# Kernel tuning notes

Hardware: AMD Instinct MI355X
Metric: run time of the kernel (lower is better)

## Reference

```python
import jax, jax.numpy as jnp
import numpy as np


def _linear_init(key, fan_in, fan_out):
    bound = 1.0 / np.sqrt(fan_in)
    k1, k2 = jax.random.split(key)
    w = jax.random.uniform(k1, (fan_in, fan_out), jnp.float32, -bound, bound)
    b = jax.random.uniform(k2, (fan_out,), jnp.float32, -bound, bound)
    return w, b


def setup_inputs() -> dict:
    key = jax.random.key(0)
    ks = jax.random.split(key, 8)
    B, T, K, F, H, D = 4, 64, 50, 6, 128, 256
    states = jax.random.normal(ks[0], (B, T, K, F), jnp.float32)
    masks = (jax.random.uniform(ks[1], (B, T, K)) < 0.9).astype(jnp.float32)
    w_a, b_a = _linear_init(ks[2], F, H)              # agent_encoder
    w_r1, b_r1 = _linear_init(ks[3], 2 * H + 3, H)    # relation_encoder layer 1
    w_r2, b_r2 = _linear_init(ks[4], H, H)            # relation_encoder layer 2
    w_g, b_g = _linear_init(ks[5], 2 * H, H)          # graph_aggregation
    w_f1, b_f1 = _linear_init(ks[6], H, D)            # final_encoder layer 1
    w_f2, b_f2 = _linear_init(ks[7], D, D)            # final_encoder layer 2
    return dict(states=states, masks=masks, w_a=w_a, b_a=b_a,
                w_r1=w_r1, b_r1=b_r1, w_r2=w_r2, b_r2=b_r2,
                w_g=w_g, b_g=b_g, w_f1=w_f1, b_f1=b_f1, w_f2=w_f2, b_f2=b_f2)


def _safe_norm(r):
    # sqrt(sum r^2) with well-defined gradient at 0 (torch.norm convention)
    sq = jnp.sum(r * r, axis=-1, keepdims=True)
    return jnp.where(sq == 0, 0.0, jnp.sqrt(jnp.where(sq == 0, 1.0, sq)))


def reference(states, masks, w_a, b_a, w_r1, b_r1, w_r2, b_r2,
              w_g, b_g, w_f1, b_f1, w_f2, b_f2):
    B, T, K, F = states.shape
    H = w_a.shape[1]
    s = states.reshape(B * T, K, F)            # [N,K,F]
    m = masks.reshape(B * T, K)                # [N,K]
    agent_feat = jax.nn.relu(s @ w_a + b_a)    # [N,K,H] (dropout = identity, eval)
    pos = s[..., :2]
    vel = s[..., 2:4]
    # rel[n,i,j] = quantity_j - quantity_i
    rel_pos = pos[:, None, :, :] - pos[:, :, None, :]   # [N,K,K,2]
    rel_vel = vel[:, None, :, :] - vel[:, :, None, :]
    dist = _safe_norm(rel_pos)                          # [N,K,K,1]
    rx, ry = rel_pos[..., 0:1], rel_pos[..., 1:2]
    safe_x = jnp.where((rx == 0) & (ry == 0), 1.0, rx)  # atan2(0,1)=atan2(0,0)=0
    angle = jnp.arctan2(ry, safe_x)
    speed_diff = _safe_norm(rel_vel)
    geo = jnp.concatenate([dist, angle, speed_diff], axis=-1)  # [N,K,K,3]
    # Split the first relation linear instead of materializing the
    # [N,K,K,2H+3] concat: cat([f_i, f_j, geo]) @ w_r1 == f@w_i + f@w_j + geo@w_geo
    x_i = agent_feat @ w_r1[:H]            # [N,K,H]
    x_j = agent_feat @ w_r1[H:2 * H]       # [N,K,H]
    g = geo @ w_r1[2 * H:] + b_r1          # [N,K,K,H]
    h = jax.nn.relu(x_i[:, :, None, :] + x_j[:, None, :, :] + g)
    rel_feat = h @ w_r2 + b_r2             # [N,K,K,H]
    mask_pairs = m[:, :, None] * m[:, None, :]          # [N,i,j]
    rel_feat = rel_feat * mask_pairs[..., None]
    denom = jnp.maximum(mask_pairs.sum(axis=2, keepdims=True), 1.0)  # [N,K,1]
    agg = rel_feat.sum(axis=2) / denom                  # [N,K,H]
    combined = jax.nn.relu(agent_feat @ w_g[:H] + agg @ w_g[H:] + b_g)  # [N,K,H]
    me = m[..., None]
    pooled = (combined * me).sum(axis=1) / jnp.maximum(me.sum(axis=1), 1.0)  # [N,H]
    latent = jax.nn.relu(pooled @ w_f1 + b_f1) @ w_f2 + b_f2                 # [N,D]
    return latent.reshape(B, T, -1)
```

## Files before the change

kernel.cpp:

```cpp
#include <hip/hip_runtime.h>

#define KA 50
#define KP 52
#define H 128
#define D 256
#define NBLK 256
#define BLOCK 1024
#define NG 8
#define RPT 7
#define STRD 136

#define WS_WI 0
#define WS_WJ 32
#define WS_WR2 64
#define WS_WG 96
#define NFRAG 160

typedef __attribute__((ext_vector_type(8))) short bf16x8;
typedef __attribute__((ext_vector_type(4))) float f32x4;

__device__ __forceinline__ float bf2f(unsigned short u) {
  return __uint_as_float(((unsigned)u) << 16);
}
__device__ __forceinline__ unsigned short f2bf(float f) {
  unsigned u = __float_as_uint(f);
  u = (u + 0x7FFFu + ((u >> 16) & 1u)) >> 16;
  return (unsigned short)u;
}
__device__ __forceinline__ float rlf(float v, int l) {
  return __int_as_float(__builtin_amdgcn_readlane(__float_as_int(v), l));
}

__global__ void pack_weights(const float* __restrict__ w_r1,
                             const float* __restrict__ w_r2,
                             const float* __restrict__ w_g,
                             unsigned short* __restrict__ wp) {
  const int t = blockIdx.x * 256 + threadIdx.x;
  if (t >= NFRAG * 64) return;
  const int f = t >> 6, lane = t & 63;
  const float* W; int rowbase, sf;
  if (f < 64)       { W = w_r1; rowbase = (f < 32) ? 0 : 128; sf = f & 31; }
  else if (f < 96)  { W = w_r2; rowbase = 0; sf = f - 64; }
  else              { W = w_g;  rowbase = 0; sf = f - 96; }
  const int kt = sf >> 3, ctl = sf & 7;
  const int col = ctl * 16 + (lane & 15);
  const int k0  = rowbase + kt * 32 + (lane >> 4) * 8;
  unsigned short v[8];
  #pragma unroll
  for (int j = 0; j < 8; ++j) v[j] = f2bf(W[(k0 + j) * H + col]);
  #pragma unroll
  for (int j = 0; j < 8; ++j) wp[(size_t)t * 8 + j] = v[j];
}

struct alignas(16) Smem {
  unsigned short af[KP * STRD];
  unsigned short xi[KP * STRD];
  unsigned short xj[KP * H];
  unsigned short hsum[KP * STRD];
  float red[1024];
  float pooled[H];
  float latent1[D];
  float s[KA][6];
  float m[64];
  float cnta[KP];
  float invden[KP];
  float cnt;
};

__global__ void __launch_bounds__(BLOCK) rpe_kernel(
    const float* __restrict__ states, const float* __restrict__ masks,
    const float* __restrict__ w_a,  const float* __restrict__ b_a,
    const float* __restrict__ w_r1, const float* __restrict__ b_r1,
    const float* __restrict__ b_r2,
    const float* __restrict__ b_g,
    const float* __restrict__ w_f1, const float* __restrict__ b_f1,
    const float* __restrict__ w_f2, const float* __restrict__ b_f2,
    const unsigned short* __restrict__ wp,
    float* __restrict__ out) {
  __shared__ Smem sh;
  const int n = blockIdx.x;
  const int tid = threadIdx.x;
  const int c = tid & (H - 1);
  const int bg = tid >> 7;
  const int wid = tid >> 6, lane = tid & 63;
  const int ct = wid & 7;
  const int rtb = (wid >> 3) * 2;
  const int fr = lane & 15;
  const int fkg = lane >> 4;
  const int col = ct * 16 + fr;

  const float bac = b_a[c];
  const float wa0 = w_a[0*H+c], wa1 = w_a[1*H+c], wa2 = w_a[2*H+c];
  const float wa3 = w_a[3*H+c], wa4 = w_a[4*H+c], wa5 = w_a[5*H+c];
  const int c0 = 2 * lane;
  const float wgd0  = w_r1[256*H + c0], wgd1  = w_r1[256*H + c0+1];
  const float wgan0 = w_r1[257*H + c0], wgan1 = w_r1[257*H + c0+1];
  const float wgs0  = w_r1[258*H + c0], wgs1  = w_r1[258*H + c0+1];
  const float br10  = b_r1[c0],         br11  = b_r1[c0+1];

  {
    if (tid < KA * 6) ((float*)sh.s)[tid] = states[(size_t)n * (KA * 6) + tid];
    if (tid < 64) sh.m[tid] = (tid < KA) ? masks[(size_t)n * KA + tid] : 0.f;
    if (tid < 2 * H) {
      const int r5 = KA + (tid >> 7), cc = tid & (H - 1);
      sh.af[r5 * STRD + cc] = 0;
      sh.hsum[r5 * STRD + cc] = 0;
    }
  }
  __syncthreads();
  if (wid == 0) {
    float v = sh.m[lane];
    v += __shfl_xor(v, 1);  v += __shfl_xor(v, 2);  v += __shfl_xor(v, 4);
    v += __shfl_xor(v, 8);  v += __shfl_xor(v, 16); v += __shfl_xor(v, 32);
    if (lane == 0) sh.cnt = v;
  }

  const int bl = (lane < KA) ? lane : (KA - 1);
  const float pbx = sh.s[bl][0], pby = sh.s[bl][1];
  const float pvx = sh.s[bl][2], pvy = sh.s[bl][3];
  const float mb  = sh.m[lane];
  float dG[3], aG[3], sG[3];
  #pragma unroll
  for (int r = 0; r < 3; ++r) {
    const int ar = wid + 16 * r;
    const float rx  = pbx - sh.s[ar][0], ry  = pby - sh.s[ar][1];
    const float dvx = pvx - sh.s[ar][2], dvy = pvy - sh.s[ar][3];
    dG[r] = sqrtf(fmaf(rx, rx, ry * ry));
    const float sx = (rx == 0.f && ry == 0.f) ? 1.f : rx;
    aG[r] = atan2f(ry, sx);
    sG[r] = sqrtf(fmaf(dvx, dvx, dvy * dvy));
  }
  float dGt = 0.f, aGt = 0.f, sGt = 0.f;
  if (wid < 2) {
    const int ar = 48 + wid;
    const float rx  = pbx - sh.s[ar][0], ry  = pby - sh.s[ar][1];
    const float dvx = pvx - sh.s[ar][2], dvy = pvy - sh.s[ar][3];
    dGt = sqrtf(fmaf(rx, rx, ry * ry));
    const float sx = (rx == 0.f && ry == 0.f) ? 1.f : rx;
    aGt = atan2f(ry, sx);
    sGt = sqrtf(fmaf(dvx, dvx, dvy * dvy));
  }

  {
    #pragma unroll
    for (int r = 0; r < RPT; ++r) {
      const int a = bg + NG * r;
      if (a < KA) {
        const float* srow = sh.s[a];
        float v = fmaf(srow[0], wa0, fmaf(srow[1], wa1, fmaf(srow[2], wa2,
                  fmaf(srow[3], wa3, fmaf(srow[4], wa4, fmaf(srow[5], wa5, bac))))));
        sh.af[a * STRD + c] = f2bf(fmaxf(v, 0.f));
      }
    }
  }
  bf16x8 Bi[4], Bj[4];
  #pragma unroll
  for (int kt = 0; kt < 4; ++kt) {
    Bi[kt] = *(const bf16x8*)&wp[(size_t)((WS_WI + kt*8 + ct) * 64 + lane) * 8];
    Bj[kt] = *(const bf16x8*)&wp[(size_t)((WS_WJ + kt*8 + ct) * 64 + lane) * 8];
  }
  __syncthreads();
  if (tid < KP) {
    const float ca = (tid < KA) ? sh.m[tid] * sh.cnt : 0.f;
    sh.cnta[tid] = ca;
    sh.invden[tid] = 1.0f / fmaxf(ca, 1.0f);
  }

  {
    f32x4 ci0 = {0,0,0,0}, ci1 = {0,0,0,0}, cj0 = {0,0,0,0}, cj1 = {0,0,0,0};
    #pragma unroll
    for (int kt = 0; kt < 4; ++kt) {
      const bf16x8 A0 = *(const bf16x8*)&sh.af[(rtb*16 + fr) * STRD + kt*32 + fkg*8];
      const bf16x8 A1 = *(const bf16x8*)&sh.af[((rtb+1)*16 + fr) * STRD + kt*32 + fkg*8];
      ci0 = __builtin_amdgcn_mfma_f32_16x16x32_bf16(A0, Bi[kt], ci0, 0, 0, 0);
      ci1 = __builtin_amdgcn_mfma_f32_16x16x32_bf16(A1, Bi[kt], ci1, 0, 0, 0);
      cj0 = __builtin_amdgcn_mfma_f32_16x16x32_bf16(A0, Bj[kt], cj0, 0, 0, 0);
      cj1 = __builtin_amdgcn_mfma_f32_16x16x32_bf16(A1, Bj[kt], cj1, 0, 0, 0);
    }
    #pragma unroll
    for (int rt2 = 0; rt2 < 2; ++rt2) {
      const f32x4 vi = rt2 ? ci1 : ci0;
      const f32x4 vj = rt2 ? cj1 : cj0;
      #pragma unroll
      for (int g = 0; g < 4; ++g) {
        const int r = (rtb + rt2) * 16 + fkg * 4 + g;
        if (r < KP) {
          sh.xi[r * STRD + col] = f2bf(vi[g]);
          sh.xj[r * H + col]    = f2bf(vj[g]);
        }
      }
    }
  }
  __syncthreads();

  {
    float b0v[3], b1v[3], h0v[3], h1v[3];
    #pragma unroll
    for (int r = 0; r < 3; ++r) {
      const int ar = wid + 16 * r;
      const unsigned xip = *(const unsigned*)&sh.xi[ar * STRD + c0];
      b0v[r] = bf2f((unsigned short)xip) + br10;
      b1v[r] = bf2f((unsigned short)(xip >> 16)) + br11;
      h0v[r] = 0.f; h1v[r] = 0.f;
    }
    #pragma unroll 10
    for (int b = 0; b < KA; ++b) {
      const unsigned xjp = *(const unsigned*)&sh.xj[b * H + c0];
      const float xj0 = __uint_as_float(xjp << 16);
      const float xj1 = __uint_as_float(xjp & 0xFFFF0000u);
      const float mm = rlf(mb, b);
      #pragma unroll
      for (int r = 0; r < 3; ++r) {
        const float dd = rlf(dG[r], b), aa = rlf(aG[r], b), ss = rlf(sG[r], b);
        float t0 = fmaf(dd, wgd0, b0v[r]); t0 = fmaf(aa, wgan0, t0);
        t0 = fmaf(ss, wgs0, t0);  t0 += xj0;
        float t1 = fmaf(dd, wgd1, b1v[r]); t1 = fmaf(aa, wgan1, t1);
        t1 = fmaf(ss, wgs1, t1);  t1 += xj1;
        h0v[r] = fmaf(mm, fmaxf(t0, 0.f), h0v[r]);
        h1v[r] = fmaf(mm, fmaxf(t1, 0.f), h1v[r]);
      }
    }
    #pragma unroll
    for (int r = 0; r < 3; ++r) {
      const int ar = wid + 16 * r;
      const float ma = sh.m[ar];
      const float g0 = h0v[r] * ma, g1 = h1v[r] * ma;
      *(unsigned*)&sh.hsum[ar * STRD + c0] =
          (unsigned)f2bf(g0) | ((unsigned)f2bf(g1) << 16);
    }
    if (wid < 2) {
      const int ar = 48 + wid;
      const unsigned xip = *(const unsigned*)&sh.xi[ar * STRD + c0];
      const float b0t = bf2f((unsigned short)xip) + br10;
      const float b1t = bf2f((unsigned short)(xip >> 16)) + br11;
      float h0 = 0.f, h1 = 0.f;
      #pragma unroll 10
      for (int b = 0; b < KA; ++b) {
        const unsigned xjp = *(const unsigned*)&sh.xj[b * H + c0];
        const float xj0 = __uint_as_float(xjp << 16);
        const float xj1 = __uint_as_float(xjp & 0xFFFF0000u);
        const float mm = rlf(mb, b);
        const float dd = rlf(dGt, b), aa = rlf(aGt, b), ss = rlf(sGt, b);
        float t0 = fmaf(dd, wgd0, b0t); t0 = fmaf(aa, wgan0, t0);
        t0 = fmaf(ss, wgs0, t0);  t0 += xj0;
        float t1 = fmaf(dd, wgd1, b1t); t1 = fmaf(aa, wgan1, t1);
        t1 = fmaf(ss, wgs1, t1);  t1 += xj1;
        h0 = fmaf(mm, fmaxf(t0, 0.f), h0);
        h1 = fmaf(mm, fmaxf(t1, 0.f), h1);
      }
      const float ma = sh.m[ar];
      const float g0 = h0 * ma, g1 = h1 * ma;
      *(unsigned*)&sh.hsum[ar * STRD + c0] =
          (unsigned)f2bf(g0) | ((unsigned)f2bf(g1) << 16);
    }
  }
  __syncthreads();

  f32x4 p0 = {0,0,0,0}, p1 = {0,0,0,0};
  {
    f32x4 a0 = {0,0,0,0}, a1 = {0,0,0,0};
    #pragma unroll
    for (int kt = 0; kt < 4; ++kt) {
      const bf16x8 B4 = *(const bf16x8*)&wp[(size_t)((WS_WR2 + kt*8 + ct) * 64 + lane) * 8];
      const bf16x8 A0h = *(const bf16x8*)&sh.hsum[(rtb*16 + fr) * STRD + kt*32 + fkg*8];
      const bf16x8 A1h = *(const bf16x8*)&sh.hsum[((rtb+1)*16 + fr) * STRD + kt*32 + fkg*8];
      a0 = __builtin_amdgcn_mfma_f32_16x16x32_bf16(A0h, B4, a0, 0, 0, 0);
      a1 = __builtin_amdgcn_mfma_f32_16x16x32_bf16(A1h, B4, a1, 0, 0, 0);
      const bf16x8 B5 = *(const bf16x8*)&wp[(size_t)((WS_WG + kt*8 + ct) * 64 + lane) * 8];
      const bf16x8 A0a = *(const bf16x8*)&sh.af[(rtb*16 + fr) * STRD + kt*32 + fkg*8];
      const bf16x8 A1a = *(const bf16x8*)&sh.af[((rtb+1)*16 + fr) * STRD + kt*32 + fkg*8];
      p0 = __builtin_amdgcn_mfma_f32_16x16x32_bf16(A0a, B5, p0, 0, 0, 0);
      p1 = __builtin_amdgcn_mfma_f32_16x16x32_bf16(A1a, B5, p1, 0, 0, 0);
    }
    const float br2c = b_r2[col];
    #pragma unroll
    for (int rt2 = 0; rt2 < 2; ++rt2) {
      const f32x4 v = rt2 ? a1 : a0;
      #pragma unroll
      for (int g = 0; g < 4; ++g) {
        const int r = (rtb + rt2) * 16 + fkg * 4 + g;
        if (r < KP) {
          const float val = fmaf(sh.cnta[r], br2c, v[g]) * sh.invden[r];
          sh.xi[r * STRD + col] = f2bf(val);
        }
      }
    }
  }
  __syncthreads();

  {
    #pragma unroll
    for (int kt = 0; kt < 4; ++kt) {
      const bf16x8 B = *(const bf16x8*)&wp[(size_t)((WS_WG + (kt+4)*8 + ct) * 64 + lane) * 8];
      const bf16x8 A0 = *(const bf16x8*)&sh.xi[(rtb*16 + fr) * STRD + kt*32 + fkg*8];
      const bf16x8 A1 = *(const bf16x8*)&sh.xi[((rtb+1)*16 + fr) * STRD + kt*32 + fkg*8];
      p0 = __builtin_amdgcn_mfma_f32_16x16x32_bf16(A0, B, p0, 0, 0, 0);
      p1 = __builtin_amdgcn_mfma_f32_16x16x32_bf16(A1, B, p1, 0, 0, 0);
    }
    const float bgc = b_g[col];
    float pv = 0.f;
    #pragma unroll
    for (int rt2 = 0; rt2 < 2; ++rt2) {
      const f32x4 v = rt2 ? p1 : p0;
      #pragma unroll
      for (int g = 0; g < 4; ++g) {
        const int r = (rtb + rt2) * 16 + fkg * 4 + g;
        if (r < KA) {
          pv = fmaf(sh.m[r], fmaxf(v[g] + bgc, 0.f), pv);
        }
      }
    }
    pv += __shfl_xor(pv, 16);
    pv += __shfl_xor(pv, 32);
    if (lane < 16) sh.red[(wid >> 3) * H + col] = pv;
  }
  const int d67 = tid & (D - 1);
  const int hh67 = tid >> 8;
  float wf1r[32];
  {
    const float* wf = w_f1 + d67;
    const int k06 = hh67 * 32;
    #pragma unroll
    for (int k = 0; k < 32; ++k) wf1r[k] = wf[(k06 + k) * D];
  }
  __syncthreads();
  if (tid < H) {
    const float invp = 1.0f / fmaxf(sh.cnt, 1.0f);
    sh.pooled[tid] = (sh.red[tid] + sh.red[H + tid]) * invp;
  }
  __syncthreads();

  {
    float acc = 0.f;
    const int k06 = hh67 * 32;
    #pragma unroll
    for (int k = 0; k < 32; ++k)
      acc = fmaf(sh.pooled[k06 + k], wf1r[k], acc);
    sh.red[hh67 * D + d67] = acc;
  }
  float wf2r[64];
  {
    const float* wf = w_f2 + d67;
    const int k07 = hh67 * 64;
    #pragma unroll
    for (int k = 0; k < 64; ++k) wf2r[k] = wf[(k07 + k) * D];
  }
  __syncthreads();
  if (tid < D) {
    sh.latent1[tid] = fmaxf(sh.red[tid] + sh.red[D + tid] +
                            sh.red[2*D + tid] + sh.red[3*D + tid] +
                            b_f1[tid], 0.f);
  }
  __syncthreads();

  {
    float acc = 0.f;
    const int k07 = hh67 * 64;
    #pragma unroll
    for (int k = 0; k < 64; ++k)
      acc = fmaf(sh.latent1[k07 + k], wf2r[k], acc);
    sh.red[hh67 * D + d67] = acc;
  }
  __syncthreads();
  if (tid < D) {
    out[(size_t)n * D + tid] = sh.red[tid] + sh.red[D + tid] +
                               sh.red[2*D + tid] + sh.red[3*D + tid] +
                               b_f2[tid];
  }
}

extern "C" void kernel_launch(void* const* d_in, const int* in_sizes, int n_in,
                              void* d_out, int out_size, void* d_ws, size_t ws_size,
                              hipStream_t stream) {
  const float* states = (const float*)d_in[0];
  const float* masks  = (const float*)d_in[1];
  const float* w_a  = (const float*)d_in[2];
  const float* b_a  = (const float*)d_in[3];
  const float* w_r1 = (const float*)d_in[4];
  const float* b_r1 = (const float*)d_in[5];
  const float* w_r2 = (const float*)d_in[6];
  const float* b_r2 = (const float*)d_in[7];
  const float* w_g  = (const float*)d_in[8];
  const float* b_g  = (const float*)d_in[9];
  const float* w_f1 = (const float*)d_in[10];
  const float* b_f1 = (const float*)d_in[11];
  const float* w_f2 = (const float*)d_in[12];
  const float* b_f2 = (const float*)d_in[13];
  float* out = (float*)d_out;
  unsigned short* wp = (unsigned short*)d_ws;

  hipLaunchKernelGGL(pack_weights, dim3((NFRAG * 64 + 255) / 256), dim3(256), 0, stream,
                     w_r1, w_r2, w_g, wp);
  hipLaunchKernelGGL(rpe_kernel, dim3(NBLK), dim3(BLOCK), 0, stream,
                     states, masks, w_a, b_a, w_r1, b_r1, b_r2,
                     b_g, w_f1, b_f1, w_f2, b_f2, wp, out);
}
```

Measured before the change: 42.59 us.

## Pack geometry into bf16 pairs, vectorize pair loop, drop weight prefetch registers

The pairwise relation loop now packs dist, angle, speed-diff and mask into two bf16-packed 32-bit values per row. That halves the readlane broadcasts per iteration (two instead of four per row), and the math is rewritten as 2-wide float vectors so the compiler can emit packed FMA/max. The final MLP no longer preloads w_f1/w_f2 columns into 32 and 64 registers ahead of barriers; it reads them from global inside partially unrolled loops. This lowers register pressure, but the geometry terms lose precision to bf16 and the weight-load latency is no longer hidden behind the barriers.

```diff
diff --git a/kernel.cpp b/kernel.cpp
--- a/kernel.cpp
+++ b/kernel.cpp
@@ -18,6 +18,7 @@
 
 typedef __attribute__((ext_vector_type(8))) short bf16x8;
 typedef __attribute__((ext_vector_type(4))) float f32x4;
+typedef __attribute__((ext_vector_type(2))) float v2f;
 
 __device__ __forceinline__ float bf2f(unsigned short u) {
   return __uint_as_float(((unsigned)u) << 16);
@@ -27,8 +28,8 @@
   u = (u + 0x7FFFu + ((u >> 16) & 1u)) >> 16;
   return (unsigned short)u;
 }
-__device__ __forceinline__ float rlf(float v, int l) {
-  return __int_as_float(__builtin_amdgcn_readlane(__float_as_int(v), l));
+__device__ __forceinline__ int rli(int v, int l) {
+  return __builtin_amdgcn_readlane(v, l);
 }
 
 __global__ void pack_weights(const float* __restrict__ w_r1,
@@ -93,10 +94,10 @@
   const float wa0 = w_a[0*H+c], wa1 = w_a[1*H+c], wa2 = w_a[2*H+c];
   const float wa3 = w_a[3*H+c], wa4 = w_a[4*H+c], wa5 = w_a[5*H+c];
   const int c0 = 2 * lane;
-  const float wgd0  = w_r1[256*H + c0], wgd1  = w_r1[256*H + c0+1];
-  const float wgan0 = w_r1[257*H + c0], wgan1 = w_r1[257*H + c0+1];
-  const float wgs0  = w_r1[258*H + c0], wgs1  = w_r1[258*H + c0+1];
-  const float br10  = b_r1[c0],         br11  = b_r1[c0+1];
+  const v2f wgd01  = { w_r1[256*H + c0], w_r1[256*H + c0+1] };
+  const v2f wgan01 = { w_r1[257*H + c0], w_r1[257*H + c0+1] };
+  const v2f wgs01  = { w_r1[258*H + c0], w_r1[258*H + c0+1] };
+  const v2f br101  = { b_r1[c0], b_r1[c0+1] };
 
   {
     if (tid < KA * 6) ((float*)sh.s)[tid] = states[(size_t)n * (KA * 6) + tid];
@@ -118,27 +119,31 @@
   const int bl = (lane < KA) ? lane : (KA - 1);
   const float pbx = sh.s[bl][0], pby = sh.s[bl][1];
   const float pvx = sh.s[bl][2], pvy = sh.s[bl][3];
-  const float mb  = sh.m[lane];
-  float dG[3], aG[3], sG[3];
+  const unsigned mbits = (sh.m[lane] != 0.f) ? 0x3F800000u : 0u;
+  unsigned q0[3], q1[3];
   #pragma unroll
   for (int r = 0; r < 3; ++r) {
     const int ar = wid + 16 * r;
     const float rx  = pbx - sh.s[ar][0], ry  = pby - sh.s[ar][1];
     const float dvx = pvx - sh.s[ar][2], dvy = pvy - sh.s[ar][3];
-    dG[r] = sqrtf(fmaf(rx, rx, ry * ry));
+    const float dist = sqrtf(fmaf(rx, rx, ry * ry));
     const float sx = (rx == 0.f && ry == 0.f) ? 1.f : rx;
-    aG[r] = atan2f(ry, sx);
-    sG[r] = sqrtf(fmaf(dvx, dvx, dvy * dvy));
-  }
-  float dGt = 0.f, aGt = 0.f, sGt = 0.f;
+    const float ang = atan2f(ry, sx);
+    const float sd  = sqrtf(fmaf(dvx, dvx, dvy * dvy));
+    q0[r] = (unsigned)f2bf(dist) | ((unsigned)f2bf(ang) << 16);
+    q1[r] = (unsigned)f2bf(sd) | mbits;
+  }
+  unsigned q0t = 0, q1t = 0;
   if (wid < 2) {
     const int ar = 48 + wid;
     const float rx  = pbx - sh.s[ar][0], ry  = pby - sh.s[ar][1];
     const float dvx = pvx - sh.s[ar][2], dvy = pvy - sh.s[ar][3];
-    dGt = sqrtf(fmaf(rx, rx, ry * ry));
+    const float dist = sqrtf(fmaf(rx, rx, ry * ry));
     const float sx = (rx == 0.f && ry == 0.f) ? 1.f : rx;
-    aGt = atan2f(ry, sx);
-    sGt = sqrtf(fmaf(dvx, dvx, dvy * dvy));
+    const float ang = atan2f(ry, sx);
+    const float sd  = sqrtf(fmaf(dvx, dvx, dvy * dvy));
+    q0t = (unsigned)f2bf(dist) | ((unsigned)f2bf(ang) << 16);
+    q1t = (unsigned)f2bf(sd) | mbits;
   }
 
   {
@@ -194,64 +199,67 @@
   __syncthreads();
 
   {
-    float b0v[3], b1v[3], h0v[3], h1v[3];
+    v2f base01[3], acc01[3];
     #pragma unroll
     for (int r = 0; r < 3; ++r) {
       const int ar = wid + 16 * r;
       const unsigned xip = *(const unsigned*)&sh.xi[ar * STRD + c0];
-      b0v[r] = bf2f((unsigned short)xip) + br10;
-      b1v[r] = bf2f((unsigned short)(xip >> 16)) + br11;
-      h0v[r] = 0.f; h1v[r] = 0.f;
+      base01[r] = (v2f){ bf2f((unsigned short)xip), bf2f((unsigned short)(xip >> 16)) } + br101;
+      acc01[r] = (v2f){0.f, 0.f};
     }
     #pragma unroll 10
     for (int b = 0; b < KA; ++b) {
       const unsigned xjp = *(const unsigned*)&sh.xj[b * H + c0];
-      const float xj0 = __uint_as_float(xjp << 16);
-      const float xj1 = __uint_as_float(xjp & 0xFFFF0000u);
-      const float mm = rlf(mb, b);
+      const v2f xj01 = { __uint_as_float(xjp << 16),
+                         __uint_as_float(xjp & 0xFFFF0000u) };
       #pragma unroll
       for (int r = 0; r < 3; ++r) {
-        const float dd = rlf(dG[r], b), aa = rlf(aG[r], b), ss = rlf(sG[r], b);
-        float t0 = fmaf(dd, wgd0, b0v[r]); t0 = fmaf(aa, wgan0, t0);
-        t0 = fmaf(ss, wgs0, t0);  t0 += xj0;
-        float t1 = fmaf(dd, wgd1, b1v[r]); t1 = fmaf(aa, wgan1, t1);
-        t1 = fmaf(ss, wgs1, t1);  t1 += xj1;
-        h0v[r] = fmaf(mm, fmaxf(t0, 0.f), h0v[r]);
-        h1v[r] = fmaf(mm, fmaxf(t1, 0.f), h1v[r]);
+        const unsigned rq0 = (unsigned)rli((int)q0[r], b);
+        const unsigned rq1 = (unsigned)rli((int)q1[r], b);
+        const float dd = __uint_as_float(rq0 << 16);
+        const float aa = __uint_as_float(rq0 & 0xFFFF0000u);
+        const float ss = __uint_as_float(rq1 << 16);
+        const float mm = __uint_as_float(rq1 & 0xFFFF0000u);
+        v2f t = __builtin_elementwise_fma((v2f){dd, dd}, wgd01, base01[r] + xj01);
+        t = __builtin_elementwise_fma((v2f){aa, aa}, wgan01, t);
+        t = __builtin_elementwise_fma((v2f){ss, ss}, wgs01, t);
+        t = __builtin_elementwise_max(t, (v2f){0.f, 0.f});
+        acc01[r] = __builtin_elementwise_fma((v2f){mm, mm}, t, acc01[r]);
       }
     }
     #pragma unroll
     for (int r = 0; r < 3; ++r) {
       const int ar = wid + 16 * r;
       const float ma = sh.m[ar];
-      const float g0 = h0v[r] * ma, g1 = h1v[r] * ma;
       *(unsigned*)&sh.hsum[ar * STRD + c0] =
-          (unsigned)f2bf(g0) | ((unsigned)f2bf(g1) << 16);
+          (unsigned)f2bf(acc01[r].x * ma) | ((unsigned)f2bf(acc01[r].y * ma) << 16);
     }
     if (wid < 2) {
       const int ar = 48 + wid;
       const unsigned xip = *(const unsigned*)&sh.xi[ar * STRD + c0];
-      const float b0t = bf2f((unsigned short)xip) + br10;
-      const float b1t = bf2f((unsigned short)(xip >> 16)) + br11;
-      float h0 = 0.f, h1 = 0.f;
+      const v2f baset = (v2f){ bf2f((unsigned short)xip),
+                               bf2f((unsigned short)(xip >> 16)) } + br101;
+      v2f acct = {0.f, 0.f};
       #pragma unroll 10
       for (int b = 0; b < KA; ++b) {
         const unsigned xjp = *(const unsigned*)&sh.xj[b * H + c0];
-        const float xj0 = __uint_as_float(xjp << 16);
-        const float xj1 = __uint_as_float(xjp & 0xFFFF0000u);
-        const float mm = rlf(mb, b);
-        const float dd = rlf(dGt, b), aa = rlf(aGt, b), ss = rlf(sGt, b);
-        float t0 = fmaf(dd, wgd0, b0t); t0 = fmaf(aa, wgan0, t0);
-        t0 = fmaf(ss, wgs0, t0);  t0 += xj0;
-        float t1 = fmaf(dd, wgd1, b1t); t1 = fmaf(aa, wgan1, t1);
-        t1 = fmaf(ss, wgs1, t1);  t1 += xj1;
-        h0 = fmaf(mm, fmaxf(t0, 0.f), h0);
-        h1 = fmaf(mm, fmaxf(t1, 0.f), h1);
+        const v2f xj01 = { __uint_as_float(xjp << 16),
+                           __uint_as_float(xjp & 0xFFFF0000u) };
+        const unsigned rq0 = (unsigned)rli((int)q0t, b);
+        const unsigned rq1 = (unsigned)rli((int)q1t, b);
+        const float dd = __uint_as_float(rq0 << 16);
+        const float aa = __uint_as_float(rq0 & 0xFFFF0000u);
+        const float ss = __uint_as_float(rq1 << 16);
+        const float mm = __uint_as_float(rq1 & 0xFFFF0000u);
+        v2f t = __builtin_elementwise_fma((v2f){dd, dd}, wgd01, baset + xj01);
+        t = __builtin_elementwise_fma((v2f){aa, aa}, wgan01, t);
+        t = __builtin_elementwise_fma((v2f){ss, ss}, wgs01, t);
+        t = __builtin_elementwise_max(t, (v2f){0.f, 0.f});
+        acct = __builtin_elementwise_fma((v2f){mm, mm}, t, acct);
       }
       const float ma = sh.m[ar];
-      const float g0 = h0 * ma, g1 = h1 * ma;
       *(unsigned*)&sh.hsum[ar * STRD + c0] =
-          (unsigned)f2bf(g0) | ((unsigned)f2bf(g1) << 16);
+          (unsigned)f2bf(acct.x * ma) | ((unsigned)f2bf(acct.y * ma) << 16);
     }
   }
   __syncthreads();
@@ -314,15 +322,6 @@
     pv += __shfl_xor(pv, 32);
     if (lane < 16) sh.red[(wid >> 3) * H + col] = pv;
   }
-  const int d67 = tid & (D - 1);
-  const int hh67 = tid >> 8;
-  float wf1r[32];
-  {
-    const float* wf = w_f1 + d67;
-    const int k06 = hh67 * 32;
-    #pragma unroll
-    for (int k = 0; k < 32; ++k) wf1r[k] = wf[(k06 + k) * D];
-  }
   __syncthreads();
   if (tid < H) {
     const float invp = 1.0f / fmaxf(sh.cnt, 1.0f);
@@ -331,19 +330,15 @@
   __syncthreads();
 
   {
+    const int d  = tid & (D - 1);
+    const int hh = tid >> 8;
+    const float* wf = w_f1 + d;
     float acc = 0.f;
-    const int k06 = hh67 * 32;
-    #pragma unroll
+    const int k0 = hh * 32;
+    #pragma unroll 8
     for (int k = 0; k < 32; ++k)
-      acc = fmaf(sh.pooled[k06 + k], wf1r[k], acc);
-    sh.red[hh67 * D + d67] = acc;
-  }
-  float wf2r[64];
-  {
-    const float* wf = w_f2 + d67;
-    const int k07 = hh67 * 64;
-    #pragma unroll
-    for (int k = 0; k < 64; ++k) wf2r[k] = wf[(k07 + k) * D];
+      acc = fmaf(sh.pooled[k0 + k], wf[(k0 + k) * D], acc);
+    sh.red[hh * D + d] = acc;
   }
   __syncthreads();
   if (tid < D) {
@@ -354,12 +349,15 @@
   __syncthreads();
 
   {
+    const int d  = tid & (D - 1);
+    const int hh = tid >> 8;
+    const float* wf = w_f2 + d;
     float acc = 0.f;
-    const int k07 = hh67 * 64;
-    #pragma unroll
+    const int k0 = hh * 64;
+    #pragma unroll 8
     for (int k = 0; k < 64; ++k)
-      acc = fmaf(sh.latent1[k07 + k], wf2r[k], acc);
-    sh.red[hh67 * D + d67] = acc;
+      acc = fmaf(sh.latent1[k0 + k], wf[(k0 + k) * D], acc);
+    sh.red[hh * D + d] = acc;
   }
   __syncthreads();
   if (tid < D) {
```

After: 37.73 us. -11.4%, faster.
